# Performance work log

Hardware: AMD Instinct MI355X
Metric: run time of the kernel (lower is better)

## Reference

```python
import jax, jax.numpy as jnp
import numpy as np

H, C_K, C_Q = 4, 512, 512


def setup_inputs() -> dict:
    key = jax.random.key(0)
    ks = jax.random.split(key, 6)
    s = 1.0 / np.sqrt(512.0)
    return {
        "x_k": jax.random.normal(ks[0], (4096, 512), jnp.float32),
        "x_q": jax.random.normal(ks[1], (4096, 512), jnp.float32),
        "k_w": jax.random.normal(ks[2], (H * C_K, 512), jnp.float32) * s,
        "q_w": jax.random.normal(ks[3], (H * C_Q, 512), jnp.float32) * s,
        "attn_w": jax.random.normal(ks[4], (H, C_K, C_Q), jnp.float32) * s,
        "proj_w": jax.random.normal(ks[5], (C_K, C_Q), jnp.float32) * s,
    }


def reference(x_k, x_q, k_w, q_w, attn_w, proj_w):
    # Project keys/queries and split into heads: [H, N, c]
    xk = (x_k @ k_w.T).reshape(-1, H, C_K).transpose(1, 0, 2)
    xq = (x_q @ q_w.T).reshape(-1, H, C_Q).transpose(1, 0, 2)
    # Bilinear scores: alphas[h, n, m] = xk[h,n,:] @ attn_w[h] @ xq[h,m,:]
    alphas = jnp.einsum("hnk,hkq,hmq->hnm", xk, attn_w, xq)
    # key-side update
    alpha_ks = jax.nn.softmax(alphas, axis=2)                 # [H, Nk, Nq]
    alpha_k_agg = jnp.mean(jnp.einsum("hnm,hmq->hnq", alpha_ks, xq), axis=0)
    x_k_update = alpha_k_agg @ proj_w.T                       # [Nk, C_K]
    # query-side update (bidirectional)
    alpha_qs = jax.nn.softmax(alphas.transpose(0, 2, 1), axis=2)  # [H, Nq, Nk]
    alpha_q_agg = jnp.mean(jnp.einsum("hmn,hnk->hmk", alpha_qs, xk), axis=0)
    x_q_update = alpha_q_agg @ proj_w                         # [Nq, C_Q]
    return x_k + x_k_update, x_q + x_q_update
```

## Files before the change

### kernel.cpp

```cpp
#include <hip/hip_runtime.h>
#include <stdint.h>

#define DEVI __device__ __forceinline__

typedef unsigned short u16;
typedef unsigned int u32;
typedef __attribute__((ext_vector_type(4))) unsigned short u16x4;
typedef __attribute__((ext_vector_type(8))) unsigned short u16x8;
typedef __attribute__((ext_vector_type(4))) float f32x4;
typedef __attribute__((ext_vector_type(8))) _Float16 f16x8;

static constexpr int NT = 4096;
static constexpr int D  = 512;
static constexpr int NH = 4;
static constexpr int KS = 4;

DEVI u16 f2h(float f) {
  _Float16 h = (_Float16)f;
  union { _Float16 h; u16 u; } v; v.h = h;
  return v.u;
}
DEVI float h2f(u16 u) {
  union { u16 u; _Float16 h; } v; v.u = u;
  return (float)v.h;
}

DEVI u32 enc_ord(float f) {
  u32 u = __float_as_uint(f);
  return (u & 0x80000000u) ? ~u : (u | 0x80000000u);
}
DEVI float dec_ord(u32 k) {
  u32 u = (k & 0x80000000u) ? (k ^ 0x80000000u) : ~k;
  return __uint_as_float(u);
}

DEVI void gld_lds16(const u16* g, u16* l) {
  __builtin_amdgcn_global_load_lds((const __attribute__((address_space(1))) void*)g,
                                   (__attribute__((address_space(3))) void*)l, 16, 0, 0);
}

enum { OUT_F32 = 0, OUT_F16 = 2, OUT_RES = 3, OUT_SMAX = 4, OUT_F16T = 5 };

template<int OUT>
__global__ __launch_bounds__(256)
void gemm_bt(const u16* __restrict__ A, int lda, size_t zsA,
             const u16* __restrict__ B, int ldb, size_t zsB,
             void* __restrict__ Cp, int ldc, size_t zsC,
             const float* __restrict__ res, const float* __restrict__ res2, int K,
             u32* __restrict__ rmg, u32* __restrict__ cmg,
             u16* __restrict__ STp, int ldct, size_t zsT)
{
  constexpr bool DOT = (OUT == OUT_SMAX || OUT == OUT_F16T);
  __shared__ u16 As[128 * 32];
  __shared__ u16 Bs[128 * 32];
  __shared__ u32 rmaxs[128], cmaxs[128];
  __shared__ u16 Tt[DOT ? 128 * 72 : 8];
  A += blockIdx.z * zsA;
  B += blockIdx.z * zsB;
  const float* resz = (OUT == OUT_RES && blockIdx.z) ? res2 : res;
  const int tid = threadIdx.x;
  const int lane = tid & 63, w = tid >> 6;
  const int wr = w >> 1, wc = w & 1;

  int m0, n0;
  if (OUT == OUT_SMAX) {
    int lid = blockIdx.x + 32 * blockIdx.y;
    int swz = (lid & 7) * 128 + (lid >> 3);
    n0 = (swz & 31) * 128;
    m0 = (swz >> 5) * 128;
  } else {
    m0 = blockIdx.y * 128;
    n0 = blockIdx.x * 128;
  }

  if (OUT == OUT_SMAX && tid < 128) { rmaxs[tid] = 0u; cmaxs[tid] = 0u; }

  f32x4 acc[4][4] = {};

  for (int k0 = 0; k0 < K; k0 += 32) {
    __syncthreads();
#pragma unroll
    for (int p = 0; p < 2; ++p) {
      int id = p * 256 + tid;
      int row = id >> 2, q = id & 3;
      gld_lds16(A + (size_t)(m0 + row) * lda + k0 + q * 8, As + id * 8);
      gld_lds16(B + (size_t)(n0 + row) * ldb + k0 + q * 8, Bs + id * 8);
    }
    __syncthreads();
    f16x8 af[4], bfv[4];
#pragma unroll
    for (int i = 0; i < 4; ++i)
      af[i] = *(const f16x8*)(As + (wr * 64 + i * 16 + (lane & 15)) * 32 + (lane >> 4) * 8);
#pragma unroll
    for (int i = 0; i < 4; ++i)
      bfv[i] = *(const f16x8*)(Bs + (wc * 64 + i * 16 + (lane & 15)) * 32 + (lane >> 4) * 8);
#pragma unroll
    for (int i = 0; i < 4; ++i)
#pragma unroll
      for (int j = 0; j < 4; ++j)
        acc[i][j] = __builtin_amdgcn_mfma_f32_16x16x32_f16(af[i], bfv[j], acc[i][j], 0, 0, 0);
  }

#pragma unroll
  for (int i = 0; i < 4; ++i) {
    int rl0 = wr * 64 + i * 16 + (lane >> 4) * 4;
#pragma unroll
    for (int j = 0; j < 4; ++j) {
      int c = n0 + wc * 64 + j * 16 + (lane & 15);
#pragma unroll
      for (int e = 0; e < 4; ++e) {
        size_t idx = blockIdx.z * zsC + (size_t)(m0 + rl0 + e) * ldc + c;
        float v = acc[i][j][e];
        if (OUT == OUT_F32) ((float*)Cp)[idx] = v;
        if (OUT == OUT_F16 || DOT) ((u16*)Cp)[idx] = f2h(v);
        if (OUT == OUT_RES) ((float*)Cp)[idx] = resz[(size_t)(m0 + rl0 + e) * ldc + c] + v;
      }
    }
  }

  if (OUT == OUT_SMAX) {
#pragma unroll
    for (int i = 0; i < 4; ++i) {
      int rl0 = wr * 64 + i * 16 + (lane >> 4) * 4;
#pragma unroll
      for (int e = 0; e < 4; ++e) {
        float m = fmaxf(fmaxf(acc[i][0][e], acc[i][1][e]), fmaxf(acc[i][2][e], acc[i][3][e]));
        atomicMax(&rmaxs[rl0 + e], enc_ord(m));
      }
    }
#pragma unroll
    for (int j = 0; j < 4; ++j) {
      float m = -3e38f;
#pragma unroll
      for (int i = 0; i < 4; ++i)
#pragma unroll
        for (int e = 0; e < 4; ++e) m = fmaxf(m, acc[i][j][e]);
      atomicMax(&cmaxs[wc * 64 + j * 16 + (lane & 15)], enc_ord(m));
    }
    __syncthreads();
    if (tid < 128) {
      atomicMax(rmg + m0 + tid, rmaxs[tid]);
      atomicMax(cmg + n0 + tid, cmaxs[tid]);
    }
  }

  if (DOT) {
#pragma unroll
    for (int half = 0; half < 2; ++half) {
      __syncthreads();
      if (wr == half) {
#pragma unroll
        for (int i = 0; i < 4; ++i) {
          int rl = i * 16 + (lane >> 4) * 4;
#pragma unroll
          for (int j = 0; j < 4; ++j) {
            int cl = wc * 64 + j * 16 + (lane & 15);
            u16x4 v;
            v[0] = f2h(acc[i][j][0]); v[1] = f2h(acc[i][j][1]);
            v[2] = f2h(acc[i][j][2]); v[3] = f2h(acc[i][j][3]);
            *(u16x4*)&Tt[cl * 72 + rl] = v;
          }
        }
      }
      __syncthreads();
#pragma unroll
      for (int q = 0; q < 4; ++q) {
        int id2 = q * 256 + tid;
        int c = id2 >> 3, mm = (id2 & 7) * 8;
        u16x8 v = *(const u16x8*)&Tt[c * 72 + mm];
        *(u16x8*)(STp + blockIdx.z * zsT + (size_t)(n0 + c) * ldct + m0 + half * 64 + mm) = v;
      }
    }
  }
}

__global__ __launch_bounds__(256)
void pv(const u16* __restrict__ Sarg, const u32* __restrict__ mx_u,
        const u16* __restrict__ B,
        u16* __restrict__ part, float* __restrict__ lpart, int Ksl)
{
  __shared__ u16 As[64 * 40];
  __shared__ u16 Bs[128 * 32];
  __shared__ float ps[4][64];
  const int tid = threadIdx.x;
  const int lane = tid & 63, w = tid >> 6;
  const int wr = w >> 1, wc = w & 1;

  const int lid = blockIdx.x + 4 * (blockIdx.y + 64 * blockIdx.z);
  const int swz = (lid & 7) * 128 + (lid >> 3);
  const int bx = swz & 3, by = (swz >> 2) & 63, bz = swz >> 8;

  const int m0 = by * 64, n0 = bx * 128;
  const int kb = bz * Ksl;

  const int rA = tid >> 2, kc = (tid & 3) * 8;
  const float mxA = dec_ord(mx_u[m0 + rA]);
  const u16* S0 = Sarg + (size_t)(m0 + rA) * NT + kb + kc;

  f32x4 acc[2][4] = {};
  float sacc = 0.f;

  f16x8 sv0 = *(const f16x8*)S0;

  for (int k0 = 0; k0 < Ksl; k0 += 32) {
    __syncthreads();
#pragma unroll
    for (int p = 0; p < 2; ++p) {
      int id = p * 256 + tid;
      int row = id >> 2, q = id & 3;
      gld_lds16(B + (size_t)(n0 + row) * NT + kb + k0 + q * 8, Bs + id * 8);
    }
    f16x8 nx0;
    if (k0 + 32 < Ksl) nx0 = *(const f16x8*)(S0 + k0 + 32);
    {
      u16x8 pk;
      float rs = 0.f;
#pragma unroll
      for (int j = 0; j < 8; ++j) {
        float e = __expf((float)sv0[j] - mxA);
        rs += e; pk[j] = f2h(e);
      }
      *(u16x8*)(As + rA * 40 + kc) = pk;
      sacc += rs;
    }
    __syncthreads();
    f16x8 af[2], bfv[4];
#pragma unroll
    for (int i = 0; i < 2; ++i)
      af[i] = *(const f16x8*)(As + (wr * 32 + i * 16 + (lane & 15)) * 40 + (lane >> 4) * 8);
#pragma unroll
    for (int j = 0; j < 4; ++j)
      bfv[j] = *(const f16x8*)(Bs + (wc * 64 + j * 16 + (lane & 15)) * 32 + (lane >> 4) * 8);
#pragma unroll
    for (int i = 0; i < 2; ++i)
#pragma unroll
      for (int j = 0; j < 4; ++j)
        acc[i][j] = __builtin_amdgcn_mfma_f32_16x16x32_f16(af[i], bfv[j], acc[i][j], 0, 0, 0);
    sv0 = nx0;
  }

  u16* out = part + (size_t)bz * NT * D;
#pragma unroll
  for (int i = 0; i < 2; ++i) {
    int r0 = m0 + wr * 32 + i * 16 + (lane >> 4) * 4;
#pragma unroll
    for (int j = 0; j < 4; ++j) {
      int c = n0 + wc * 64 + j * 16 + (lane & 15);
#pragma unroll
      for (int e = 0; e < 4; ++e)
        out[(size_t)(r0 + e) * D + c] = f2h(acc[i][j][e]);
    }
  }

  __syncthreads();
  ps[tid & 3][tid >> 2] = sacc;
  __syncthreads();
  if (bx == 0 && tid < 64) {
    lpart[(size_t)bz * NT + m0 + tid] =
        ps[0][tid] + ps[1][tid] + ps[2][tid] + ps[3][tid];
  }
}

__global__ __launch_bounds__(256)
void reduce2(const u16* __restrict__ pk, const float* __restrict__ lk,
             const u16* __restrict__ pq, const float* __restrict__ lq,
             u16* __restrict__ a0h, u16* __restrict__ a1h)
{
  const size_t i = ((size_t)blockIdx.x * 256 + threadIdx.x) * 4;
  const int m = (int)(i >> 9);
  const size_t zs = (size_t)NT * D;
  float Lk = 0.f, Lq = 0.f;
#pragma unroll
  for (int z = 0; z < KS; ++z) { Lk += lk[(size_t)z * NT + m]; Lq += lq[(size_t)z * NT + m]; }
  float s0 = 0.f, s1 = 0.f, s2 = 0.f, s3 = 0.f;
#pragma unroll
  for (int z = 0; z < KS; ++z) {
    u16x4 v = *(const u16x4*)(pk + z * zs + i);
    s0 += h2f(v[0]); s1 += h2f(v[1]); s2 += h2f(v[2]); s3 += h2f(v[3]);
  }
  float ck = 0.25f / Lk;
  u16x4 a = *(const u16x4*)(a0h + i);
  u16x4 na;
  na[0] = f2h(h2f(a[0]) + s0 * ck); na[1] = f2h(h2f(a[1]) + s1 * ck);
  na[2] = f2h(h2f(a[2]) + s2 * ck); na[3] = f2h(h2f(a[3]) + s3 * ck);
  *(u16x4*)(a0h + i) = na;
  s0 = s1 = s2 = s3 = 0.f;
#pragma unroll
  for (int z = 0; z < KS; ++z) {
    u16x4 v = *(const u16x4*)(pq + z * zs + i);
    s0 += h2f(v[0]); s1 += h2f(v[1]); s2 += h2f(v[2]); s3 += h2f(v[3]);
  }
  float cq = 0.25f / Lq;
  u16x4 b = *(const u16x4*)(a1h + i);
  u16x4 nb;
  nb[0] = f2h(h2f(b[0]) + s0 * cq); nb[1] = f2h(h2f(b[1]) + s1 * cq);
  nb[2] = f2h(h2f(b[2]) + s2 * cq); nb[3] = f2h(h2f(b[3]) + s3 * cq);
  *(u16x4*)(a1h + i) = nb;
}

__global__ __launch_bounds__(256)
void cast_multi(const float* p0, const float* p1, const float* p2,
                const float* p3, const float* p4, const float* p5,
                u16* o0, u16* o1, u16* o2, u16* o3, u16* o4, u16* o5,
                int n0, int n1, int n2, int n3, int n4, int n5)
{
  const float* in; u16* out; int n;
  switch (blockIdx.z) {
    case 0: in = p0; out = o0; n = n0; break;
    case 1: in = p1; out = o1; n = n1; break;
    case 2: in = p2; out = o2; n = n2; break;
    case 3: in = p3; out = o3; n = n3; break;
    case 4: in = p4; out = o4; n = n4; break;
    default: in = p5; out = o5; n = n5; break;
  }
  int i = (blockIdx.x * 256 + threadIdx.x) * 8;
  if (i >= n) return;
  f32x4 a = *(const f32x4*)(in + i), b = *(const f32x4*)(in + i + 4);
  u16x8 s;
  s[0] = f2h(a[0]); s[1] = f2h(a[1]); s[2] = f2h(a[2]); s[3] = f2h(a[3]);
  s[4] = f2h(b[0]); s[5] = f2h(b[1]); s[6] = f2h(b[2]); s[7] = f2h(b[3]);
  *(u16x8*)(out + i) = s;
}

__global__ __launch_bounds__(256)
void transpose_cast_f32(const float* __restrict__ in, int ldi,
                        u16* __restrict__ out, int ldo)
{
  __shared__ u16 t[64][72];
  int r0 = blockIdx.x * 64, c0 = blockIdx.y * 64;
  int t8 = threadIdx.x & 7, rr = threadIdx.x >> 3;
#pragma unroll
  for (int p = 0; p < 2; ++p) {
    int r = rr + p * 32;
    const float* src = in + (size_t)(r0 + r) * ldi + c0 + t8 * 8;
    f32x4 a = *(const f32x4*)src, b = *(const f32x4*)(src + 4);
    u16x8 s;
    s[0] = f2h(a[0]); s[1] = f2h(a[1]); s[2] = f2h(a[2]); s[3] = f2h(a[3]);
    s[4] = f2h(b[0]); s[5] = f2h(b[1]); s[6] = f2h(b[2]); s[7] = f2h(b[3]);
    *(u16x8*)&t[r][t8 * 8] = s;
  }
  __syncthreads();
#pragma unroll
  for (int p = 0; p < 2; ++p) {
    int c = rr + p * 32;
    u16x8 s;
#pragma unroll
    for (int j = 0; j < 8; ++j) s[j] = t[t8 * 8 + j][c];
    *(u16x8*)(out + (size_t)(c0 + c) * ldo + r0 + t8 * 8) = s;
  }
}

extern "C" void kernel_launch(void* const* d_in, const int* in_sizes, int n_in,
                              void* d_out, int out_size, void* d_ws, size_t ws_size,
                              hipStream_t stream)
{
  const float* x_k    = (const float*)d_in[0];
  const float* x_q    = (const float*)d_in[1];
  const float* k_w    = (const float*)d_in[2];
  const float* q_w    = (const float*)d_in[3];
  const float* attn_w = (const float*)d_in[4];
  const float* proj_w = (const float*)d_in[5];
  float* out0 = (float*)d_out;
  float* out1 = out0 + (size_t)NT * D;

  char* wptr = (char*)d_ws;
  auto alloc = [&](size_t bytes) { char* p = wptr; wptr += (bytes + 255) & ~(size_t)255; return p; };
  u16*   pb     = (u16*)  alloc((size_t)D * D * 2);
  u16*   pbT    = (u16*)  alloc((size_t)D * D * 2);
  u16*   XKall  = (u16*)  alloc((size_t)NT * NH * D * 2);
  u16*   XKTall = (u16*)  alloc((size_t)NT * NH * D * 2);
  u16*   XQTall = (u16*)  alloc((size_t)NT * NH * D * 2);
  u16*   Kpall  = (u16*)  alloc((size_t)NH * NT * D * 2);
  u16*   partK  = (u16*)  alloc((size_t)KS * NT * D * 2);
  u16*   partQ  = (u16*)  alloc((size_t)KS * NT * D * 2);
  u16*   agg0h  = (u16*)  alloc((size_t)NT * D * 2);
  u16*   agg1h  = (u16*)  alloc((size_t)NT * D * 2);
  float* lk     = (float*)alloc((size_t)KS * NT * 4);
  float* lq     = (float*)alloc((size_t)KS * NT * 4);
  u32*   rowm_u = (u32*)  alloc((size_t)NT * 4);
  u32*   colm_u = (u32*)  alloc((size_t)NT * 4);
  u16*   ST     = (u16*)  alloc((size_t)NT * NT * 2);
  char*  Sreg   = alloc((size_t)NT * NT * 2);
  u16*   S      = (u16*)Sreg;
  char* sp = Sreg;
  auto salloc = [&](size_t bytes) { char* p = sp; sp += (bytes + 255) & ~(size_t)255; return p; };
  u16* xkb   = (u16*)salloc((size_t)NT * D * 2);
  u16* xqb   = (u16*)salloc((size_t)NT * D * 2);
  u16* kwb   = (u16*)salloc((size_t)NH * D * D * 2);
  u16* qwb   = (u16*)salloc((size_t)NH * D * D * 2);
  u16* Abf   = (u16*)salloc((size_t)NH * D * D * 2);
  u16* XQall = (u16*)salloc((size_t)NT * NH * D * 2);

  cast_multi<<<dim3(NT * D / 2048, 1, 6), 256, 0, stream>>>(
      x_k, x_q, k_w, q_w, attn_w, proj_w,
      xkb, xqb, kwb, qwb, Abf, pb,
      NT * D, NT * D, NH * D * D, NH * D * D, NH * D * D, D * D);
  transpose_cast_f32<<<dim3(D / 64, D / 64), 256, 0, stream>>>(proj_w, D, pbT, D);

  gemm_bt<OUT_F16T><<<dim3(NH * D / 128, NT / 128, 2), 256, 0, stream>>>(
      xkb, D, (size_t)(xqb - xkb), kwb, D, (size_t)(qwb - kwb),
      XKall, NH * D, (size_t)(XQall - XKall), nullptr, nullptr, D,
      nullptr, nullptr, XKTall, NT, (size_t)(XQTall - XKTall));
  gemm_bt<OUT_F16><<<dim3(D / 128, NT / 128, NH), 256, 0, stream>>>(
      XQall, NH * D, (size_t)D, Abf, D, (size_t)D * D, Kpall, D, (size_t)NT * D,
      nullptr, nullptr, D, nullptr, nullptr, nullptr, 0, 0);

  hipMemsetAsync(agg0h, 0, (size_t)2 * NT * D * 2, stream);

  for (int h = 0; h < NH; ++h) {
    const u16* XKh  = XKall + (size_t)h * D;
    const u16* XKTh = XKTall + (size_t)h * D * NT;
    const u16* XQTh = XQTall + (size_t)h * D * NT;
    const u16* Kph  = Kpall + (size_t)h * NT * D;

    hipMemsetAsync(rowm_u, 0, (size_t)NT * 4 * 2, stream);

    gemm_bt<OUT_SMAX><<<dim3(NT / 128, NT / 128), 256, 0, stream>>>(
        XKh, NH * D, 0, Kph, D, 0, S, NT, 0, nullptr, nullptr, D,
        rowm_u, colm_u, ST, NT, 0);

    pv<<<dim3(D / 128, NT / 64, KS), 256, 0, stream>>>(
        S, rowm_u, XQTh, partK, lk, NT / KS);
    pv<<<dim3(D / 128, NT / 64, KS), 256, 0, stream>>>(
        ST, colm_u, XKTh, partQ, lq, NT / KS);

    reduce2<<<NT * D / 1024, 256, 0, stream>>>(partK, lk, partQ, lq, agg0h, agg1h);
  }

  gemm_bt<OUT_RES><<<dim3(D / 128, NT / 128, 2), 256, 0, stream>>>(
      agg0h, D, (size_t)(agg1h - agg0h), pb, D, (size_t)(pbT - pb),
      out0, D, (size_t)NT * D, x_k, x_q, D, nullptr, nullptr, nullptr, 0, 0);
}
```

Baseline: 561.3 us.

## Shrink pv tile to 32 rows, drop block swizzles, hoist max-buffer memsets

```diff
diff --git a/kernel.cpp b/kernel.cpp
--- a/kernel.cpp
+++ b/kernel.cpp
@@ -8,6 +8,7 @@
 typedef __attribute__((ext_vector_type(4))) unsigned short u16x4;
 typedef __attribute__((ext_vector_type(8))) unsigned short u16x8;
 typedef __attribute__((ext_vector_type(4))) float f32x4;
+typedef __attribute__((ext_vector_type(4))) _Float16 f16x4;
 typedef __attribute__((ext_vector_type(8))) _Float16 f16x8;
 
 static constexpr int NT = 4096;
@@ -61,17 +62,7 @@
   const int tid = threadIdx.x;
   const int lane = tid & 63, w = tid >> 6;
   const int wr = w >> 1, wc = w & 1;
-
-  int m0, n0;
-  if (OUT == OUT_SMAX) {
-    int lid = blockIdx.x + 32 * blockIdx.y;
-    int swz = (lid & 7) * 128 + (lid >> 3);
-    n0 = (swz & 31) * 128;
-    m0 = (swz >> 5) * 128;
-  } else {
-    m0 = blockIdx.y * 128;
-    n0 = blockIdx.x * 128;
-  }
+  const int m0 = blockIdx.y * 128, n0 = blockIdx.x * 128;
 
   if (OUT == OUT_SMAX && tid < 128) { rmaxs[tid] = 0u; cmaxs[tid] = 0u; }
 
@@ -179,28 +170,27 @@
         const u16* __restrict__ B,
         u16* __restrict__ part, float* __restrict__ lpart, int Ksl)
 {
-  __shared__ u16 As[64 * 40];
+  __shared__ u16 As[32 * 40];
   __shared__ u16 Bs[128 * 32];
-  __shared__ float ps[4][64];
+  __shared__ float ps[8][32];
   const int tid = threadIdx.x;
   const int lane = tid & 63, w = tid >> 6;
-  const int wr = w >> 1, wc = w & 1;
-
-  const int lid = blockIdx.x + 4 * (blockIdx.y + 64 * blockIdx.z);
-  const int swz = (lid & 7) * 128 + (lid >> 3);
-  const int bx = swz & 3, by = (swz >> 2) & 63, bz = swz >> 8;
-
-  const int m0 = by * 64, n0 = bx * 128;
+
+  const int lid = blockIdx.x + 4 * (blockIdx.y + 128 * blockIdx.z);
+  const int swz = (lid & 7) * 256 + (lid >> 3);
+  const int bx = swz & 3, by = (swz >> 2) & 127, bz = swz >> 9;
+
+  const int m0 = by * 32, n0 = bx * 128;
   const int kb = bz * Ksl;
 
-  const int rA = tid >> 2, kc = (tid & 3) * 8;
+  const int rA = tid >> 3, kc4 = (tid & 7) * 4;
   const float mxA = dec_ord(mx_u[m0 + rA]);
-  const u16* S0 = Sarg + (size_t)(m0 + rA) * NT + kb + kc;
-
-  f32x4 acc[2][4] = {};
+  const u16* S0 = Sarg + (size_t)(m0 + rA) * NT + kb + kc4;
+
+  f32x4 acc[2][2] = {};
   float sacc = 0.f;
 
-  f16x8 sv0 = *(const f16x8*)S0;
+  f16x4 sv0 = *(const f16x4*)S0;
 
   for (int k0 = 0; k0 < Ksl; k0 += 32) {
     __syncthreads();
@@ -210,31 +200,31 @@
       int row = id >> 2, q = id & 3;
       gld_lds16(B + (size_t)(n0 + row) * NT + kb + k0 + q * 8, Bs + id * 8);
     }
-    f16x8 nx0;
-    if (k0 + 32 < Ksl) nx0 = *(const f16x8*)(S0 + k0 + 32);
+    f16x4 nx0;
+    if (k0 + 32 < Ksl) nx0 = *(const f16x4*)(S0 + k0 + 32);
     {
-      u16x8 pk;
+      u16x4 pk;
       float rs = 0.f;
 #pragma unroll
-      for (int j = 0; j < 8; ++j) {
+      for (int j = 0; j < 4; ++j) {
         float e = __expf((float)sv0[j] - mxA);
         rs += e; pk[j] = f2h(e);
       }
-      *(u16x8*)(As + rA * 40 + kc) = pk;
+      *(u16x4*)(As + rA * 40 + kc4) = pk;
       sacc += rs;
     }
     __syncthreads();
-    f16x8 af[2], bfv[4];
+    f16x8 af[2], bfv[2];
 #pragma unroll
     for (int i = 0; i < 2; ++i)
-      af[i] = *(const f16x8*)(As + (wr * 32 + i * 16 + (lane & 15)) * 40 + (lane >> 4) * 8);
-#pragma unroll
-    for (int j = 0; j < 4; ++j)
-      bfv[j] = *(const f16x8*)(Bs + (wc * 64 + j * 16 + (lane & 15)) * 32 + (lane >> 4) * 8);
+      af[i] = *(const f16x8*)(As + (i * 16 + (lane & 15)) * 40 + (lane >> 4) * 8);
+#pragma unroll
+    for (int j = 0; j < 2; ++j)
+      bfv[j] = *(const f16x8*)(Bs + (w * 32 + j * 16 + (lane & 15)) * 32 + (lane >> 4) * 8);
 #pragma unroll
     for (int i = 0; i < 2; ++i)
 #pragma unroll
-      for (int j = 0; j < 4; ++j)
+      for (int j = 0; j < 2; ++j)
         acc[i][j] = __builtin_amdgcn_mfma_f32_16x16x32_f16(af[i], bfv[j], acc[i][j], 0, 0, 0);
     sv0 = nx0;
   }
@@ -242,10 +232,10 @@
   u16* out = part + (size_t)bz * NT * D;
 #pragma unroll
   for (int i = 0; i < 2; ++i) {
-    int r0 = m0 + wr * 32 + i * 16 + (lane >> 4) * 4;
-#pragma unroll
-    for (int j = 0; j < 4; ++j) {
-      int c = n0 + wc * 64 + j * 16 + (lane & 15);
+    int r0 = m0 + i * 16 + (lane >> 4) * 4;
+#pragma unroll
+    for (int j = 0; j < 2; ++j) {
+      int c = n0 + w * 32 + j * 16 + (lane & 15);
 #pragma unroll
       for (int e = 0; e < 4; ++e)
         out[(size_t)(r0 + e) * D + c] = f2h(acc[i][j][e]);
@@ -253,11 +243,13 @@
   }
 
   __syncthreads();
-  ps[tid & 3][tid >> 2] = sacc;
+  ps[tid & 7][tid >> 3] = sacc;
   __syncthreads();
-  if (bx == 0 && tid < 64) {
-    lpart[(size_t)bz * NT + m0 + tid] =
-        ps[0][tid] + ps[1][tid] + ps[2][tid] + ps[3][tid];
+  if (bx == 0 && tid < 32) {
+    float s = 0.f;
+#pragma unroll
+    for (int g = 0; g < 8; ++g) s += ps[g][tid];
+    lpart[(size_t)bz * NT + m0 + tid] = s;
   }
 }
 
@@ -377,8 +369,8 @@
   u16*   agg1h  = (u16*)  alloc((size_t)NT * D * 2);
   float* lk     = (float*)alloc((size_t)KS * NT * 4);
   float* lq     = (float*)alloc((size_t)KS * NT * 4);
-  u32*   rowm_u = (u32*)  alloc((size_t)NT * 4);
-  u32*   colm_u = (u32*)  alloc((size_t)NT * 4);
+  u32*   rowm_u = (u32*)  alloc((size_t)NH * NT * 4);
+  u32*   colm_u = (u32*)  alloc((size_t)NH * NT * 4);
   u16*   ST     = (u16*)  alloc((size_t)NT * NT * 2);
   char*  Sreg   = alloc((size_t)NT * NT * 2);
   u16*   S      = (u16*)Sreg;
@@ -406,23 +398,24 @@
       nullptr, nullptr, D, nullptr, nullptr, nullptr, 0, 0);
 
   hipMemsetAsync(agg0h, 0, (size_t)2 * NT * D * 2, stream);
+  hipMemsetAsync(rowm_u, 0, (size_t)2 * NH * NT * 4, stream);
 
   for (int h = 0; h < NH; ++h) {
     const u16* XKh  = XKall + (size_t)h * D;
     const u16* XKTh = XKTall + (size_t)h * D * NT;
     const u16* XQTh = XQTall + (size_t)h * D * NT;
     const u16* Kph  = Kpall + (size_t)h * NT * D;
-
-    hipMemsetAsync(rowm_u, 0, (size_t)NT * 4 * 2, stream);
+    u32* rmh = rowm_u + (size_t)h * NT;
+    u32* cmh = colm_u + (size_t)h * NT;
 
     gemm_bt<OUT_SMAX><<<dim3(NT / 128, NT / 128), 256, 0, stream>>>(
         XKh, NH * D, 0, Kph, D, 0, S, NT, 0, nullptr, nullptr, D,
-        rowm_u, colm_u, ST, NT, 0);
-
-    pv<<<dim3(D / 128, NT / 64, KS), 256, 0, stream>>>(
-        S, rowm_u, XQTh, partK, lk, NT / KS);
-    pv<<<dim3(D / 128, NT / 64, KS), 256, 0, stream>>>(
-        ST, colm_u, XKTh, partQ, lq, NT / KS);
+        rmh, cmh, ST, NT, 0);
+
+    pv<<<dim3(D / 128, NT / 32, KS), 256, 0, stream>>>(
+        S, rmh, XQTh, partK, lk, NT / KS);
+    pv<<<dim3(D / 128, NT / 32, KS), 256, 0, stream>>>(
+        ST, cmh, XKTh, partQ, lq, NT / KS);
 
     reduce2<<<NT * D / 1024, 256, 0, stream>>>(partK, lk, partQ, lq, agg0h, agg1h);
   }
```

New measurement: 658.7 us. +17.3%, slower.
